# Optimization experiments

Measured on AMD Instinct MI355X. Metric: run time of the kernel, lower is better.

Reference implementation:

```python
import jax, jax.numpy as jnp
import numpy as np

B, S, H = 16, 2048, 1024

def setup_inputs() -> dict:
    key = jax.random.key(0)
    k1, k2, k3, k4, k5 = jax.random.split(key, 5)
    hidden = jax.random.normal(k1, (B, 1, H), dtype=jnp.float32)
    encoder_outputs = jax.random.normal(k2, (B, S, H), dtype=jnp.float32)
    # nn.Linear(2H -> H): weight [H, 2H], bias [H]
    lim = 1.0 / np.sqrt(2 * H)
    attn_w = jax.random.uniform(k3, (H, 2 * H), minval=-lim, maxval=lim, dtype=jnp.float32)
    attn_b = jax.random.uniform(k4, (H,), minval=-lim, maxval=lim, dtype=jnp.float32)
    v = jax.random.normal(k5, (1, H), dtype=jnp.float32)
    return {"hidden": hidden, "encoder_outputs": encoder_outputs,
            "attn_w": attn_w, "attn_b": attn_b, "v": v}

def reference(hidden, encoder_outputs, attn_w, attn_b, v):
    # hidden: [B,1,H] broadcast across seq; encoder_outputs: [B,S,H]
    Bc, Sc, Hc = encoder_outputs.shape
    h = jnp.broadcast_to(hidden, (Bc, Sc, Hc))
    x = jnp.concatenate([h, encoder_outputs], axis=-1)        # [B,S,2H]
    energy = jnp.einsum('bsk,hk->bsh', x, attn_w) + attn_b    # [B,S,H]
    scores = jnp.einsum('bsh,h->bs', energy, v[0])            # [B,S]
    return jax.nn.softmax(scores, axis=-1)[:, None, :]        # [B,1,S]
```

## Files before the change

### kernel.cpp

```cpp
#include <hip/hip_runtime.h>
#include <math.h>

#define BATCH 16
#define SEQ   2048
#define HID   1024

__global__ __launch_bounds__(256) void we_fused_kernel(
    const float* __restrict__ attn_w,
    const float* __restrict__ v,
    float* __restrict__ w2)
{
    const int tid   = threadIdx.x;
    const int chunk = blockIdx.x;
    const int h0    = chunk * 8;

    float4 acc = make_float4(0.f, 0.f, 0.f, 0.f);
#pragma unroll
    for (int r = 0; r < 8; ++r) {
        const int h = h0 + r;
        const float vh = v[h];
        const float4 a =
            ((const float4*)(attn_w + (size_t)h * (2 * HID) + HID))[tid];
        acc.x += vh * a.x;
        acc.y += vh * a.y;
        acc.z += vh * a.z;
        acc.w += vh * a.w;
    }
    float* dst = w2 + tid * 4;
    atomicAdd(dst + 0, acc.x);
    atomicAdd(dst + 1, acc.y);
    atomicAdd(dst + 2, acc.z);
    atomicAdd(dst + 3, acc.w);
}

__global__ __launch_bounds__(256) void scores_kernel(
    const float* __restrict__ enc,
    const float* __restrict__ w2,
    float* __restrict__ scores)
{
    const int wave = (int)((blockIdx.x * 256 + threadIdx.x) >> 6);
    const int lane = threadIdx.x & 63;

    float4 w[4];
#pragma unroll
    for (int c = 0; c < 4; ++c)
        w[c] = ((const float4*)w2)[c * 64 + lane];

#pragma unroll
    for (int i = 0; i < 4; ++i) {
        const int row = wave * 4 + i;
        const float4* rp = (const float4*)(enc + (size_t)row * HID);
        float acc = 0.f;
#pragma unroll
        for (int c = 0; c < 4; ++c) {
            const float4 e = rp[c * 64 + lane];
            acc += e.x * w[c].x + e.y * w[c].y + e.z * w[c].z + e.w * w[c].w;
        }
#pragma unroll
        for (int off = 32; off > 0; off >>= 1)
            acc += __shfl_down(acc, off, 64);
        if (lane == 0)
            scores[row] = acc;
    }
}

__global__ __launch_bounds__(256) void softmax_kernel(
    const float* __restrict__ scores,
    float* __restrict__ out)
{
    const int b   = blockIdx.x;
    const int tid = threadIdx.x;
    const float* s = scores + (size_t)b * SEQ;

    __shared__ float red[256];

    float local[8];
    float m = -INFINITY;
#pragma unroll
    for (int i = 0; i < 8; ++i) {
        local[i] = s[tid + i * 256];
        m = fmaxf(m, local[i]);
    }
    red[tid] = m;
    __syncthreads();
    for (int st = 128; st > 0; st >>= 1) {
        if (tid < st) red[tid] = fmaxf(red[tid], red[tid + st]);
        __syncthreads();
    }
    m = red[0];
    __syncthreads();

    float e[8];
    float sum = 0.f;
#pragma unroll
    for (int i = 0; i < 8; ++i) {
        e[i] = __expf(local[i] - m);
        sum += e[i];
    }
    red[tid] = sum;
    __syncthreads();
    for (int st = 128; st > 0; st >>= 1) {
        if (tid < st) red[tid] += red[tid + st];
        __syncthreads();
    }
    const float inv = 1.f / red[0];
#pragma unroll
    for (int i = 0; i < 8; ++i)
        out[(size_t)b * SEQ + tid + i * 256] = e[i] * inv;
}

extern "C" void kernel_launch(void* const* d_in, const int* in_sizes, int n_in,
                              void* d_out, int out_size, void* d_ws, size_t ws_size,
                              hipStream_t stream)
{
    const float* enc    = (const float*)d_in[1];
    const float* attn_w = (const float*)d_in[2];
    const float* v      = (const float*)d_in[4];

    float* ws      = (float*)d_ws;
    float* w2      = ws;
    float* scores  = ws + HID + 128 * HID;

    hipMemsetAsync(w2, 0, HID * sizeof(float), stream);
    we_fused_kernel<<<128,  256, 0, stream>>>(attn_w, v, w2);
    scores_kernel  <<<2048, 256, 0, stream>>>(enc, w2, scores);
    softmax_kernel <<<BATCH, 256, 0, stream>>>(scores, (float*)d_out);
}
```

Baseline: 220.1 us.

## Fuse all stages into one cooperative kernel and replace atomics with partial reduction

Merges the weight-vector projection, the reduction, the score GEMV and the softmax into a single cooperative kernel separated by grid-wide syncs. This removes the memset and the multiple kernel launches. Atomic accumulation into w2 is replaced by per-block partial sums and a separate reduction pass. A fallback multi-kernel path is used if the cooperative launch fails. The trade-off is the grid-sync cost and the requirement that all 1024 blocks be co-resident.

```diff
diff --git a/kernel.cpp b/kernel.cpp
--- a/kernel.cpp
+++ b/kernel.cpp
@@ -1,14 +1,129 @@
 #include <hip/hip_runtime.h>
+#include <hip/hip_cooperative_groups.h>
 #include <math.h>
+
+namespace cg = cooperative_groups;
 
 #define BATCH 16
 #define SEQ   2048
 #define HID   1024
 
-__global__ __launch_bounds__(256) void we_fused_kernel(
+__global__ __launch_bounds__(256, 4) void fused_all_kernel(
     const float* __restrict__ attn_w,
     const float* __restrict__ v,
-    float* __restrict__ w2)
+    const float* __restrict__ enc,
+    float* __restrict__ ws,
+    float* __restrict__ out)
+{
+    cg::grid_group grid = cg::this_grid();
+    const int tid = threadIdx.x;
+    const int bid = blockIdx.x;
+
+    float* w2      = ws;
+    float* partial = ws + HID;
+    float* scores  = ws + HID + 128 * HID;
+
+    __shared__ float red[256];
+
+    if (bid < 128) {
+        const int h0 = bid * 8;
+        float4 acc = make_float4(0.f, 0.f, 0.f, 0.f);
+#pragma unroll
+        for (int r = 0; r < 8; ++r) {
+            const int h = h0 + r;
+            const float vh = v[h];
+            const float4 a =
+                ((const float4*)(attn_w + (size_t)h * (2 * HID) + HID))[tid];
+            acc.x += vh * a.x;
+            acc.y += vh * a.y;
+            acc.z += vh * a.z;
+            acc.w += vh * a.w;
+        }
+        ((float4*)(partial + (size_t)bid * HID))[tid] = acc;
+    }
+    grid.sync();
+
+    if (bid < 4) {
+        const int j = bid * 256 + tid;
+        float a = 0.f;
+#pragma unroll 8
+        for (int y = 0; y < 128; ++y)
+            a += partial[(size_t)y * HID + j];
+        w2[j] = a;
+    }
+    grid.sync();
+
+    {
+        const int wave = (bid * 256 + tid) >> 6;
+        const int lane = tid & 63;
+
+        float4 w[4];
+#pragma unroll
+        for (int c = 0; c < 4; ++c)
+            w[c] = ((const float4*)w2)[c * 64 + lane];
+
+#pragma unroll
+        for (int i = 0; i < 8; ++i) {
+            const int row = wave * 8 + i;
+            const float4* rp = (const float4*)(enc + (size_t)row * HID);
+            float acc = 0.f;
+#pragma unroll
+            for (int c = 0; c < 4; ++c) {
+                const float4 e = rp[c * 64 + lane];
+                acc += e.x * w[c].x + e.y * w[c].y + e.z * w[c].z + e.w * w[c].w;
+            }
+#pragma unroll
+            for (int off = 32; off > 0; off >>= 1)
+                acc += __shfl_down(acc, off, 64);
+            if (lane == 0)
+                scores[row] = acc;
+        }
+    }
+    grid.sync();
+
+    if (bid < BATCH) {
+        const float* s = scores + (size_t)bid * SEQ;
+
+        float local[8];
+        float m = -INFINITY;
+#pragma unroll
+        for (int i = 0; i < 8; ++i) {
+            local[i] = s[tid + i * 256];
+            m = fmaxf(m, local[i]);
+        }
+        red[tid] = m;
+        __syncthreads();
+        for (int st = 128; st > 0; st >>= 1) {
+            if (tid < st) red[tid] = fmaxf(red[tid], red[tid + st]);
+            __syncthreads();
+        }
+        m = red[0];
+        __syncthreads();
+
+        float e[8];
+        float sum = 0.f;
+#pragma unroll
+        for (int i = 0; i < 8; ++i) {
+            e[i] = __expf(local[i] - m);
+            sum += e[i];
+        }
+        red[tid] = sum;
+        __syncthreads();
+        for (int st = 128; st > 0; st >>= 1) {
+            if (tid < st) red[tid] += red[tid + st];
+            __syncthreads();
+        }
+        const float inv = 1.f / red[0];
+#pragma unroll
+        for (int i = 0; i < 8; ++i)
+            out[(size_t)bid * SEQ + tid + i * 256] = e[i] * inv;
+    }
+}
+
+__global__ __launch_bounds__(256) void we_partial_kernel(
+    const float* __restrict__ attn_w,
+    const float* __restrict__ v,
+    float* __restrict__ partial)
 {
     const int tid   = threadIdx.x;
     const int chunk = blockIdx.x;
@@ -26,11 +141,19 @@
         acc.z += vh * a.z;
         acc.w += vh * a.w;
     }
-    float* dst = w2 + tid * 4;
-    atomicAdd(dst + 0, acc.x);
-    atomicAdd(dst + 1, acc.y);
-    atomicAdd(dst + 2, acc.z);
-    atomicAdd(dst + 3, acc.w);
+    ((float4*)(partial + (size_t)chunk * HID))[tid] = acc;
+}
+
+__global__ __launch_bounds__(256) void we_reduce_kernel(
+    const float* __restrict__ partial,
+    float* __restrict__ w2)
+{
+    const int j = blockIdx.x * 256 + threadIdx.x;
+    float acc = 0.f;
+#pragma unroll 8
+    for (int y = 0; y < 128; ++y)
+        acc += partial[(size_t)y * HID + j];
+    w2[j] = acc;
 }
 
 __global__ __launch_bounds__(256) void scores_kernel(
@@ -117,12 +240,21 @@
     const float* attn_w = (const float*)d_in[2];
     const float* v      = (const float*)d_in[4];
 
-    float* ws      = (float*)d_ws;
-    float* w2      = ws;
-    float* scores  = ws + HID + 128 * HID;
-
-    hipMemsetAsync(w2, 0, HID * sizeof(float), stream);
-    we_fused_kernel<<<128,  256, 0, stream>>>(attn_w, v, w2);
-    scores_kernel  <<<2048, 256, 0, stream>>>(enc, w2, scores);
-    softmax_kernel <<<BATCH, 256, 0, stream>>>(scores, (float*)d_out);
-}
+    float* ws     = (float*)d_ws;
+    float* outp   = (float*)d_out;
+
+    void* args[] = {(void*)&attn_w, (void*)&v, (void*)&enc,
+                    (void*)&ws, (void*)&outp};
+    hipError_t err = hipLaunchCooperativeKernel(
+        (const void*)fused_all_kernel, dim3(1024), dim3(256), args, 0, stream);
+
+    if (err != hipSuccess) {
+        float* w2      = ws;
+        float* partial = ws + HID;
+        float* scores  = ws + HID + 128 * HID;
+        we_partial_kernel<<<128,  256, 0, stream>>>(attn_w, v, partial);
+        we_reduce_kernel <<<4,    256, 0, stream>>>(partial, w2);
+        scores_kernel    <<<2048, 256, 0, stream>>>(enc, w2, scores);
+        softmax_kernel   <<<BATCH, 256, 0, stream>>>(scores, outp);
+    }
+}
```

New measurement: 507.9 us. +130.8%, slower.

## Replace atomic w2 reduction with partial-sum kernel and batch row loads in scores

Applied to the files above, without the earlier changes.

Collapsing W and v into a single vector w2 was previously done with float atomics into a memset buffer. That step now writes per-chunk partial vectors and sums them in a small second kernel, removing the memset and the atomic contention. This adds a launch and 512KB of extra traffic. The scores kernel also issues loads for all four rows before reducing, using xor shuffles, to raise memory-level parallelism on the dominant 128MB encoder read.

```diff
diff --git a/kernel.cpp b/kernel.cpp
--- a/kernel.cpp
+++ b/kernel.cpp
@@ -5,10 +5,10 @@
 #define SEQ   2048
 #define HID   1024
 
-__global__ __launch_bounds__(256) void we_fused_kernel(
+__global__ __launch_bounds__(256) void we_partial_kernel(
     const float* __restrict__ attn_w,
     const float* __restrict__ v,
-    float* __restrict__ w2)
+    float* __restrict__ partial)
 {
     const int tid   = threadIdx.x;
     const int chunk = blockIdx.x;
@@ -26,11 +26,19 @@
         acc.z += vh * a.z;
         acc.w += vh * a.w;
     }
-    float* dst = w2 + tid * 4;
-    atomicAdd(dst + 0, acc.x);
-    atomicAdd(dst + 1, acc.y);
-    atomicAdd(dst + 2, acc.z);
-    atomicAdd(dst + 3, acc.w);
+    ((float4*)(partial + (size_t)chunk * HID))[tid] = acc;
+}
+
+__global__ __launch_bounds__(256) void we_reduce_kernel(
+    const float* __restrict__ partial,
+    float* __restrict__ w2)
+{
+    const int j = blockIdx.x * 256 + threadIdx.x;
+    float acc = 0.f;
+#pragma unroll 8
+    for (int y = 0; y < 128; ++y)
+        acc += partial[(size_t)y * HID + j];
+    w2[j] = acc;
 }
 
 __global__ __launch_bounds__(256) void scores_kernel(
@@ -46,21 +54,36 @@
     for (int c = 0; c < 4; ++c)
         w[c] = ((const float4*)w2)[c * 64 + lane];
 
+    float a0 = 0.f, a1 = 0.f, a2 = 0.f, a3 = 0.f;
+    const float4* rp0 = (const float4*)(enc + (size_t)(wave * 4 + 0) * HID);
+    const float4* rp1 = (const float4*)(enc + (size_t)(wave * 4 + 1) * HID);
+    const float4* rp2 = (const float4*)(enc + (size_t)(wave * 4 + 2) * HID);
+    const float4* rp3 = (const float4*)(enc + (size_t)(wave * 4 + 3) * HID);
+
 #pragma unroll
-    for (int i = 0; i < 4; ++i) {
-        const int row = wave * 4 + i;
-        const float4* rp = (const float4*)(enc + (size_t)row * HID);
-        float acc = 0.f;
+    for (int c = 0; c < 4; ++c) {
+        const float4 e0 = rp0[c * 64 + lane];
+        const float4 e1 = rp1[c * 64 + lane];
+        const float4 e2 = rp2[c * 64 + lane];
+        const float4 e3 = rp3[c * 64 + lane];
+        a0 += e0.x * w[c].x + e0.y * w[c].y + e0.z * w[c].z + e0.w * w[c].w;
+        a1 += e1.x * w[c].x + e1.y * w[c].y + e1.z * w[c].z + e1.w * w[c].w;
+        a2 += e2.x * w[c].x + e2.y * w[c].y + e2.z * w[c].z + e2.w * w[c].w;
+        a3 += e3.x * w[c].x + e3.y * w[c].y + e3.z * w[c].z + e3.w * w[c].w;
+    }
+
 #pragma unroll
-        for (int c = 0; c < 4; ++c) {
-            const float4 e = rp[c * 64 + lane];
-            acc += e.x * w[c].x + e.y * w[c].y + e.z * w[c].z + e.w * w[c].w;
-        }
-#pragma unroll
-        for (int off = 32; off > 0; off >>= 1)
-            acc += __shfl_down(acc, off, 64);
-        if (lane == 0)
-            scores[row] = acc;
+    for (int off = 32; off > 0; off >>= 1) {
+        a0 += __shfl_xor(a0, off, 64);
+        a1 += __shfl_xor(a1, off, 64);
+        a2 += __shfl_xor(a2, off, 64);
+        a3 += __shfl_xor(a3, off, 64);
+    }
+
+    if (lane < 4) {
+        const float val = (lane == 0) ? a0 : (lane == 1) ? a1
+                        : (lane == 2) ? a2 : a3;
+        scores[wave * 4 + lane] = val;
     }
 }
 
@@ -119,10 +142,11 @@
 
     float* ws      = (float*)d_ws;
     float* w2      = ws;
+    float* partial = ws + HID;
     float* scores  = ws + HID + 128 * HID;
 
-    hipMemsetAsync(w2, 0, HID * sizeof(float), stream);
-    we_fused_kernel<<<128,  256, 0, stream>>>(attn_w, v, w2);
-    scores_kernel  <<<2048, 256, 0, stream>>>(enc, w2, scores);
-    softmax_kernel <<<BATCH, 256, 0, stream>>>(scores, (float*)d_out);
+    we_partial_kernel<<<128, 256, 0, stream>>>(attn_w, v, partial);
+    we_reduce_kernel <<<4,   256, 0, stream>>>(partial, w2);
+    scores_kernel    <<<2048, 256, 0, stream>>>(enc, w2, scores);
+    softmax_kernel   <<<BATCH, 256, 0, stream>>>(scores, (float*)d_out);
 }
```

Result: faster. 214.9 us (-2.4%).
